# Kernel tuning notes

Measured on AMD Instinct MI355X. Metric: run time of the kernel, lower is better.

## Reference

```python
import jax, jax.numpy as jnp
import numpy as np

HEADS = 4
DIM_HEAD = 32
EPS = 1e-5


def setup_inputs() -> dict:
    key = jax.random.key(0)
    ks = jax.random.split(key, 3)
    b, c, h, w = 32, 128, 128, 128
    hidden = HEADS * DIM_HEAD  # 128
    x = jax.random.normal(ks[0], (b, c, h, w), dtype=jnp.float32)
    Wqkv = jax.random.normal(ks[1], (3 * hidden, c), dtype=jnp.float32) * (1.0 / np.sqrt(c))
    Wout = jax.random.normal(ks[2], (c, hidden), dtype=jnp.float32) * (1.0 / np.sqrt(hidden))
    bout = jnp.zeros((c,), dtype=jnp.float32)
    g = jnp.ones((c,), dtype=jnp.float32)
    return {"x": x, "Wqkv": Wqkv, "Wout": Wout, "bout": bout, "g": g}


def reference(x, Wqkv, Wout, bout, g):
    b, c, h, w = x.shape
    n = h * w
    scale = DIM_HEAD ** -0.5
    # 1x1 conv (no bias) == channel GEMM
    qkv = jnp.einsum('oc,bchw->bohw', Wqkv, x)  # [b, 3*hidden, h, w]
    q, k, v = jnp.split(qkv, 3, axis=1)
    # b (h d) x y -> b h d n
    def to_heads(t):
        return t.reshape(b, HEADS, DIM_HEAD, n)
    q, k, v = to_heads(q), to_heads(k), to_heads(v)
    q = jax.nn.softmax(q, axis=-2) * scale   # softmax over per-head channel dim
    k = jax.nn.softmax(k, axis=-1)           # softmax over token dim
    v = v / n
    ctx = jnp.einsum('bhdn,bhen->bhde', k, v)   # [b, heads, d, e]
    out = jnp.einsum('bhde,bhdn->bhen', ctx, q)  # [b, heads, e, n]
    out = out.reshape(b, HEADS * DIM_HEAD, h, w)
    # output 1x1 conv with bias
    y = jnp.einsum('oc,bchw->bohw', Wout, out) + bout[None, :, None, None]
    # LayerNorm over channel dim (biased variance)
    mean = jnp.mean(y, axis=1, keepdims=True)
    var = jnp.var(y, axis=1, keepdims=True)
    return (y - mean) * jax.lax.rsqrt(var + EPS) * g[None, :, None, None]
```

## Files before the change

kernel.cpp:

```cpp
#include <hip/hip_runtime.h>
#include <math.h>


#define NCHUNK 64

typedef __attribute__((ext_vector_type(8))) short short8;
typedef __attribute__((ext_vector_type(4))) float f32x4;

__device__ __forceinline__ uint bf16r(float f) {
    uint u = __float_as_uint(f);
    return (u + 0x7FFFu + ((u >> 16) & 1u)) >> 16;
}
__device__ __forceinline__ float bf16f(uint h) { return __uint_as_float(h << 16); }
__device__ __forceinline__ uint2 bsplit(float f) {
    uint h = bf16r(f);
    float r = f - bf16f(h);
    return make_uint2(h, bf16r(r));
}
__device__ __forceinline__ uint2 bsplit_t(float f) {
    uint u = __float_as_uint(f);
    uint uh = u & 0xFFFF0000u;
    float r = f - __uint_as_float(uh);
    return make_uint2(uh >> 16, __float_as_uint(r) >> 16);
}
__device__ __forceinline__ uint bpack_t(float f) {
    uint u = __float_as_uint(f);
    uint uh = u & 0xFFFF0000u;
    float r = f - __uint_as_float(uh);
    return (uh >> 16) | (__float_as_uint(r) & 0xFFFF0000u);
}
__device__ __forceinline__ short8 lo8(uint4 a, uint4 b) {
    uint4 r;
    r.x = (a.x & 0xFFFFu) | (a.y << 16);
    r.y = (a.z & 0xFFFFu) | (a.w << 16);
    r.z = (b.x & 0xFFFFu) | (b.y << 16);
    r.w = (b.z & 0xFFFFu) | (b.w << 16);
    return __builtin_bit_cast(short8, r);
}
__device__ __forceinline__ short8 hi8(uint4 a, uint4 b) {
    uint4 r;
    r.x = (a.x >> 16) | (a.y & 0xFFFF0000u);
    r.y = (a.z >> 16) | (a.w & 0xFFFF0000u);
    r.z = (b.x >> 16) | (b.y & 0xFFFF0000u);
    r.w = (b.z >> 16) | (b.w & 0xFFFF0000u);
    return __builtin_bit_cast(short8, r);
}

__global__ __launch_bounds__(256)
void wsplit(const float* __restrict__ W, ushort* __restrict__ Wh,
            ushort* __restrict__ Wl, int n)
{
    const int base = (blockIdx.x * 256 + threadIdx.x) * 4;
    if (base + 3 < n) {
        const float4 f = *(const float4*)(W + base);
        const uint2 a = bsplit(f.x), b2 = bsplit(f.y), c = bsplit(f.z), d = bsplit(f.w);
        ushort4 hh; hh.x = (ushort)a.x; hh.y = (ushort)b2.x; hh.z = (ushort)c.x; hh.w = (ushort)d.x;
        ushort4 ll; ll.x = (ushort)a.y; ll.y = (ushort)b2.y; ll.z = (ushort)c.y; ll.w = (ushort)d.y;
        *(ushort4*)(Wh + base) = hh;
        *(ushort4*)(Wl + base) = ll;
    }
}

#define MFMA(A, B, C) __builtin_amdgcn_mfma_f32_16x16x32_bf16((A), (B), (C), 0, 0, 0)

__global__ __launch_bounds__(512, 1)
void la_k1(const float* __restrict__ x,
           const ushort* __restrict__ Wh, const ushort* __restrict__ Wl,
           float* __restrict__ Spart, float* __restrict__ Zpart)
{
    __shared__ __align__(16) char smb[163840];

    const int tid = threadIdx.x;
    const int b = blockIdx.y, chunk = blockIdx.x;
    const int w = tid >> 6, l = tid & 63;
    const int l15 = l & 15, lg = l >> 4;

    {
#pragma unroll
        for (int it = 0; it < 16; ++it) {
            const int q = tid + 512 * it;
            const int region = q >> 12;
            const int lin = (q & 4095) * 16;
            const int r = lin >> 8;
            const int dst = (region << 16) + (lin ^ ((r & 7) << 4));
            const ushort* src = (region ? Wl : Wh) + 128 * 128 + (lin >> 1);
            *(uint4*)(&smb[dst]) = *(const uint4*)src;
        }
    }

    f32x4 s2[2];
#pragma unroll
    for (int i = 0; i < 2; ++i) s2[i] = (f32x4){0.f, 0.f, 0.f, 0.f};
    float zrow[4];
#pragma unroll
    for (int i = 0; i < 4; ++i) zrow[i] = 0.f;

    const int hh = w >> 1, eh = w & 1;

    for (int t = 0; t < 8; ++t) {
        const int p0 = chunk * 256 + t * 32;
        {
            const float* xb = x + (size_t)b * 128 * 16384 + p0;
            const int cp = tid >> 3, j = tid & 7;
            const int pb = j * 4, c = cp * 2;
            const float4 a = *(const float4*)(xb + (size_t)c * 16384 + pb);
            const float4 bq = *(const float4*)(xb + (size_t)(c + 1) * 16384 + pb);
            const float av[4] = {a.x, a.y, a.z, a.w};
            const float bv[4] = {bq.x, bq.y, bq.z, bq.w};
#pragma unroll
            for (int pp = 0; pp < 4; ++pp) {
                const uint2 s0 = bsplit_t(av[pp]);
                const uint2 s1 = bsplit_t(bv[pp]);
                const int p = pb + pp;
                const int byt = (p * 256 + c * 2) ^ (((p ^ (p >> 3)) & 7) << 4);
                *(uint*)(&smb[131072 + byt])        = s0.x | (s1.x << 16);
                *(uint*)(&smb[131072 + 8192 + byt]) = s0.y | (s1.y << 16);
            }
        }
        __syncthreads();

        f32x4 acc[2][2];
#pragma unroll
        for (int rt = 0; rt < 2; ++rt)
#pragma unroll
            for (int ct = 0; ct < 2; ++ct) acc[rt][ct] = (f32x4){0.f, 0.f, 0.f, 0.f};
#pragma unroll
        for (int ks = 0; ks < 4; ++ks) {
            short8 Bh[2], Bl[2];
#pragma unroll
            for (int ct = 0; ct < 2; ++ct) {
                const int p = ct * 16 + l15;
                const int byt = (p * 256 + (ks * 32 + lg * 8) * 2) ^ (((p ^ (p >> 3)) & 7) << 4);
                Bh[ct] = *(const short8*)(&smb[131072 + byt]);
                Bl[ct] = *(const short8*)(&smb[131072 + 8192 + byt]);
            }
#pragma unroll
            for (int rt = 0; rt < 2; ++rt) {
                const int r = (w + rt * 8) * 16 + l15;
                const int abyt = (r * 256 + (ks * 32 + lg * 8) * 2) ^ ((r & 7) << 4);
                const short8 Ah_ = *(const short8*)(&smb[abyt]);
                const short8 Al_ = *(const short8*)(&smb[65536 + abyt]);
#pragma unroll
                for (int ct = 0; ct < 2; ++ct) {
                    acc[rt][ct] = MFMA(Ah_, Bh[ct], acc[rt][ct]);
                    acc[rt][ct] = MFMA(Ah_, Bl[ct], acc[rt][ct]);
                    acc[rt][ct] = MFMA(Al_, Bh[ct], acc[rt][ct]);
                }
            }
        }
        __syncthreads();

#pragma unroll
        for (int rt = 0; rt < 2; ++rt) {
            const bool isk = (rt == 0);
#pragma unroll
            for (int ct = 0; ct < 2; ++ct) {
                const int p = ct * 16 + l15;
#pragma unroll
                for (int i = 0; i < 4; ++i) {
                    float val = acc[rt][ct][i];
                    if (isk) {
                        val = expf(val);
                        zrow[i] += val;
                    }
                    const int r = w * 16 + lg * 4 + i;
                    const int byt = (r * 128 + p * 4) ^ ((r & 7) << 4);
                    *(uint*)(&smb[131072 + (isk ? 0 : 16384) + byt]) = bpack_t(val);
                }
            }
        }
        __syncthreads();

        {
            short8 A2h[2], A2l[2], B2h, B2l;
#pragma unroll
            for (int rt2 = 0; rt2 < 2; ++rt2) {
                const int r = hh * 32 + rt2 * 16 + l15;
                const int b0 = (r * 128 + lg * 32) ^ ((r & 7) << 4);
                const int b1 = (r * 128 + lg * 32 + 16) ^ ((r & 7) << 4);
                const uint4 q0 = *(const uint4*)(&smb[131072 + b0]);
                const uint4 q1 = *(const uint4*)(&smb[131072 + b1]);
                A2h[rt2] = lo8(q0, q1);
                A2l[rt2] = hi8(q0, q1);
            }
            {
                const int rv = hh * 32 + eh * 16 + l15;
                const int c0 = (rv * 128 + lg * 32) ^ ((rv & 7) << 4);
                const int c1 = (rv * 128 + lg * 32 + 16) ^ ((rv & 7) << 4);
                const uint4 r0 = *(const uint4*)(&smb[131072 + 16384 + c0]);
                const uint4 r1 = *(const uint4*)(&smb[131072 + 16384 + c1]);
                B2h = lo8(r0, r1);
                B2l = hi8(r0, r1);
            }
#pragma unroll
            for (int rt2 = 0; rt2 < 2; ++rt2) {
                s2[rt2] = MFMA(A2h[rt2], B2h, s2[rt2]);
                s2[rt2] = MFMA(A2h[rt2], B2l, s2[rt2]);
                s2[rt2] = MFMA(A2l[rt2], B2h, s2[rt2]);
            }
        }
        __syncthreads();
    }

    const size_t sbase = (((size_t)b * NCHUNK + chunk) * 4 + hh) * 1024;
#pragma unroll
    for (int rt2 = 0; rt2 < 2; ++rt2)
#pragma unroll
        for (int i = 0; i < 4; ++i) {
            const int d = rt2 * 16 + lg * 4 + i;
            const int e = eh * 16 + l15;
            Spart[sbase + d * 32 + e] = s2[rt2][i];
        }

#pragma unroll
    for (int i = 0; i < 4; ++i) {
        float z = zrow[i];
        z += __shfl_xor(z, 1, 64);
        z += __shfl_xor(z, 2, 64);
        z += __shfl_xor(z, 4, 64);
        z += __shfl_xor(z, 8, 64);
        if (l15 == 0)
            Zpart[((size_t)b * NCHUNK + chunk) * 128 + w * 16 + lg * 4 + i] = z;
    }
}

__global__ __launch_bounds__(256, 1)
void la_k1_reduce(const float* __restrict__ Spart, const float* __restrict__ Zpart,
                  float* __restrict__ ctxF)
{
    const int tid = threadIdx.x;
    const int b  = blockIdx.x >> 2;
    const int hh = blockIdx.x & 3;
    const int d  = tid >> 3;
    const int e0 = (tid & 7) << 2;
    float sx = 0.f, sy = 0.f, sz = 0.f, sw = 0.f, z = 0.f;
    for (int ch = 0; ch < NCHUNK; ++ch) {
        const size_t base = (((size_t)b * NCHUNK + ch) * 4 + hh) * 32 + d;
        const float4 v = *(const float4*)(Spart + base * 32 + e0);
        sx += v.x; sy += v.y; sz += v.z; sw += v.w;
        z += Zpart[base];
    }
    const float inv = 1.0f / (z * 16384.0f);
    float4 r; r.x = sx * inv; r.y = sy * inv; r.z = sz * inv; r.w = sw * inv;
    *(float4*)(ctxF + ((((size_t)b * 4 + hh) * 32 + d) << 5) + e0) = r;
}

__global__ __launch_bounds__(256, 1)
void la_mk(const float* __restrict__ Wout, const float* __restrict__ ctxF,
           ushort* __restrict__ Mh, ushort* __restrict__ Ml)
{
    __shared__ float ctxs[4096];
    const int b = blockIdx.x;
    const int tid = threadIdx.x;
#pragma unroll
    for (int i = 0; i < 4; ++i) {
        const int idx = (tid + 256 * i) * 4;
        *(float4*)(ctxs + idx) = *(const float4*)(ctxF + (size_t)b * 4096 + idx);
    }
    __syncthreads();
    const int cp = tid & 127;
    const int dh = tid >> 7;
#pragma unroll
    for (int hq = 0; hq < 2; ++hq) {
        const int h = dh * 2 + hq;
        float wrow[32];
#pragma unroll
        for (int e4 = 0; e4 < 8; ++e4) {
            const float4 wv = *(const float4*)(Wout + cp * 128 + h * 32 + e4 * 4);
            wrow[e4 * 4 + 0] = wv.x; wrow[e4 * 4 + 1] = wv.y;
            wrow[e4 * 4 + 2] = wv.z; wrow[e4 * 4 + 3] = wv.w;
        }
        for (int d = 0; d < 32; ++d) {
            float m = 0.f;
#pragma unroll
            for (int e = 0; e < 32; ++e)
                m += wrow[e] * ctxs[h * 1024 + d * 32 + e];
            const uint2 s = bsplit(m);
            const size_t mo = (size_t)b * 16384 + cp * 128 + h * 32 + d;
            Mh[mo] = (ushort)s.x;
            Ml[mo] = (ushort)s.y;
        }
    }
}

__device__ __forceinline__ int xswz64(int p, int cbyte) {
    return (p * 256 + cbyte) ^ (((p ^ (p >> 3)) & 7) << 4);
}
__device__ __forceinline__ int qswz(int p, int off) {
    return (p * 64 + off) ^ (((p >> 1) & 3) << 4);
}

__global__ __launch_bounds__(256, 4)
void la_k2(const float* __restrict__ x,
           const ushort* __restrict__ Wqh, const ushort* __restrict__ Wql,
           const ushort* __restrict__ Mh, const ushort* __restrict__ Ml,
           const float* __restrict__ bout, const float* __restrict__ g,
           float* __restrict__ outg)
{
    __shared__ __align__(16) char smb[33792];

    const int tid = threadIdx.x;
    const int b = blockIdx.y, chunk = blockIdx.x;
    const int p0 = chunk * 64;
    const int w = tid >> 6, l = tid & 63;
    const int l15 = l & 15, lg = l >> 4;
    const int ch2 = w >> 1;
    const int rp  = w & 1;

    short8 AqH[2][4], AqL[2][4];
#pragma unroll
    for (int t_ = 0; t_ < 2; ++t_)
#pragma unroll
        for (int ks = 0; ks < 4; ++ks) {
            const size_t aoff = (size_t)((2 * w + t_) * 16 + l15) * 128 + ks * 32 + lg * 8;
            AqH[t_][ks] = *(const short8*)(Wqh + aoff);
            AqL[t_][ks] = *(const short8*)(Wql + aoff);
        }

    {
        const float* xb = x + (size_t)b * 128 * 16384 + p0;
        const int j = tid & 15, gq = tid >> 4;
        const int pb = j * 4;
#pragma unroll
        for (int u = 0; u < 2; ++u) {
            const int cb = gq * 4 + u * 64;
            const float4 xv0 = *(const float4*)(xb + (size_t)(cb + 0) * 16384 + pb);
            const float4 xv1 = *(const float4*)(xb + (size_t)(cb + 1) * 16384 + pb);
            const float4 xv2 = *(const float4*)(xb + (size_t)(cb + 2) * 16384 + pb);
            const float4 xv3 = *(const float4*)(xb + (size_t)(cb + 3) * 16384 + pb);
            float rc[4][4];
            rc[0][0] = xv0.x; rc[0][1] = xv0.y; rc[0][2] = xv0.z; rc[0][3] = xv0.w;
            rc[1][0] = xv1.x; rc[1][1] = xv1.y; rc[1][2] = xv1.z; rc[1][3] = xv1.w;
            rc[2][0] = xv2.x; rc[2][1] = xv2.y; rc[2][2] = xv2.z; rc[2][3] = xv2.w;
            rc[3][0] = xv3.x; rc[3][1] = xv3.y; rc[3][2] = xv3.z; rc[3][3] = xv3.w;
#pragma unroll
            for (int pp = 0; pp < 4; ++pp) {
                const uint2 s0 = bsplit_t(rc[0][pp]);
                const uint2 s1 = bsplit_t(rc[1][pp]);
                const uint2 s2u = bsplit_t(rc[2][pp]);
                const uint2 s3 = bsplit_t(rc[3][pp]);
                const int p = pb + pp;
                const int byt = xswz64(p, cb * 2);
                *(uint2*)(&smb[byt])         = make_uint2(s0.x | (s1.x << 16), s2u.x | (s3.x << 16));
                *(uint2*)(&smb[16384 + byt]) = make_uint2(s0.y | (s1.y << 16), s2u.y | (s3.y << 16));
            }
        }
    }
    __syncthreads();

    f32x4 qacc[2][4];
#pragma unroll
    for (int t_ = 0; t_ < 2; ++t_)
#pragma unroll
        for (int ct = 0; ct < 4; ++ct) qacc[t_][ct] = (f32x4){0.f, 0.f, 0.f, 0.f};
#pragma unroll
    for (int ks = 0; ks < 4; ++ks) {
#pragma unroll
        for (int ct = 0; ct < 4; ++ct) {
            const int p = ct * 16 + l15;
            const int byt = xswz64(p, (ks * 32 + lg * 8) * 2);
            const short8 Bh_ = *(const short8*)(&smb[byt]);
            const short8 Bl_ = *(const short8*)(&smb[16384 + byt]);
#pragma unroll
            for (int t_ = 0; t_ < 2; ++t_) {
                qacc[t_][ct] = MFMA(AqH[t_][ks], Bh_, qacc[t_][ct]);
                qacc[t_][ct] = MFMA(AqH[t_][ks], Bl_, qacc[t_][ct]);
                qacc[t_][ct] = MFMA(AqL[t_][ks], Bh_, qacc[t_][ct]);
            }
        }
    }

    float vv[4][2][4];
#pragma unroll
    for (int ct = 0; ct < 4; ++ct) {
        float m = -1e30f;
#pragma unroll
        for (int t_ = 0; t_ < 2; ++t_)
#pragma unroll
            for (int i = 0; i < 4; ++i) {
                vv[ct][t_][i] = qacc[t_][ct][i];
                m = fmaxf(m, vv[ct][t_][i]);
            }
        m = fmaxf(m, __shfl_xor(m, 16, 64));
        m = fmaxf(m, __shfl_xor(m, 32, 64));
        float s = 0.f;
#pragma unroll
        for (int t_ = 0; t_ < 2; ++t_)
#pragma unroll
            for (int i = 0; i < 4; ++i) {
                vv[ct][t_][i] = expf(vv[ct][t_][i] - m);
                s += vv[ct][t_][i];
            }
        s += __shfl_xor(s, 16, 64);
        s += __shfl_xor(s, 32, 64);
        const float inv = 0.17677669529663687f / s;
#pragma unroll
        for (int t_ = 0; t_ < 2; ++t_)
#pragma unroll
            for (int i = 0; i < 4; ++i) vv[ct][t_][i] *= inv;
    }
    __syncthreads();

#pragma unroll
    for (int ct = 0; ct < 4; ++ct) {
        const int p = ct * 16 + l15;
#pragma unroll
        for (int t_ = 0; t_ < 2; ++t_) {
            const uint2 a0 = bsplit_t(vv[ct][t_][0]);
            const uint2 a1 = bsplit_t(vv[ct][t_][1]);
            const uint2 a2 = bsplit_t(vv[ct][t_][2]);
            const uint2 a3 = bsplit_t(vv[ct][t_][3]);
            const int byt = w * 4096 + qswz(p, (t_ * 16 + lg * 4) * 2);
            *(uint2*)(&smb[byt])         = make_uint2(a0.x | (a1.x << 16), a2.x | (a3.x << 16));
            *(uint2*)(&smb[16384 + byt]) = make_uint2(a0.y | (a1.y << 16), a2.y | (a3.y << 16));
        }
    }
    __syncthreads();

    f32x4 yacc[4][2];
#pragma unroll
    for (int jj = 0; jj < 4; ++jj)
#pragma unroll
        for (int ct = 0; ct < 2; ++ct) yacc[jj][ct] = (f32x4){0.f, 0.f, 0.f, 0.f};
#pragma unroll
    for (int ks = 0; ks < 4; ++ks) {
        short8 Bh[2], Bl[2];
#pragma unroll
        for (int ct = 0; ct < 2; ++ct) {
            const int p = ch2 * 32 + ct * 16 + l15;
            const int byt = ks * 4096 + qswz(p, lg * 16);
            Bh[ct] = *(const short8*)(&smb[byt]);
            Bl[ct] = *(const short8*)(&smb[16384 + byt]);
        }
#pragma unroll
        for (int jj = 0; jj < 4; ++jj) {
            const int T = rp + 2 * jj;
            const size_t aoff = (size_t)b * 16384 + (size_t)(T * 16 + l15) * 128 + ks * 32 + lg * 8;
            const short8 Ah_ = *(const short8*)(Mh + aoff);
            const short8 Al_ = *(const short8*)(Ml + aoff);
#pragma unroll
            for (int ct = 0; ct < 2; ++ct) {
                yacc[jj][ct] = MFMA(Ah_, Bh[ct], yacc[jj][ct]);
                yacc[jj][ct] = MFMA(Ah_, Bl[ct], yacc[jj][ct]);
                yacc[jj][ct] = MFMA(Al_, Bh[ct], yacc[jj][ct]);
            }
        }
    }

    float4 bo[4], gv[4];
#pragma unroll
    for (int jj = 0; jj < 4; ++jj) {
        const int rbase = (rp + 2 * jj) * 16 + lg * 4;
        bo[jj] = *(const float4*)(bout + rbase);
        gv[jj] = *(const float4*)(g + rbase);
    }
#pragma unroll
    for (int jj = 0; jj < 4; ++jj)
#pragma unroll
        for (int ct = 0; ct < 2; ++ct) {
            yacc[jj][ct][0] += bo[jj].x;
            yacc[jj][ct][1] += bo[jj].y;
            yacc[jj][ct][2] += bo[jj].z;
            yacc[jj][ct][3] += bo[jj].w;
        }
    float* lnred = (float*)(smb + 32768);
    float sm[2], sq[2];
#pragma unroll
    for (int ct = 0; ct < 2; ++ct) {
        float s = 0.f, q = 0.f;
#pragma unroll
        for (int jj = 0; jj < 4; ++jj)
#pragma unroll
            for (int i = 0; i < 4; ++i) {
                const float yv = yacc[jj][ct][i];
                s += yv; q += yv * yv;
            }
        s += __shfl_xor(s, 16, 64); q += __shfl_xor(q, 16, 64);
        s += __shfl_xor(s, 32, 64); q += __shfl_xor(q, 32, 64);
        sm[ct] = s; sq[ct] = q;
    }
    if (lg == 0) {
#pragma unroll
        for (int ct = 0; ct < 2; ++ct) {
            const int p = ch2 * 32 + ct * 16 + l15;
            lnred[(p * 2 + rp) * 2 + 0] = sm[ct];
            lnred[(p * 2 + rp) * 2 + 1] = sq[ct];
        }
    }
    __syncthreads();
#pragma unroll
    for (int ct = 0; ct < 2; ++ct) {
        const int p = ch2 * 32 + ct * 16 + l15;
        const float st = lnred[(p * 2 + 0) * 2 + 0] + lnred[(p * 2 + 1) * 2 + 0];
        const float qt = lnred[(p * 2 + 0) * 2 + 1] + lnred[(p * 2 + 1) * 2 + 1];
        const float mean = st * (1.0f / 128.0f);
        const float var  = qt * (1.0f / 128.0f) - mean * mean;
        const float rstd = 1.0f / sqrtf(var + 1e-5f);
#pragma unroll
        for (int jj = 0; jj < 4; ++jj) {
            const int rbase = (rp + 2 * jj) * 16 + lg * 4;
            const float gg[4] = {gv[jj].x, gv[jj].y, gv[jj].z, gv[jj].w};
#pragma unroll
            for (int i = 0; i < 4; ++i) {
                const float val = (yacc[jj][ct][i] - mean) * rstd * gg[i];
                outg[((size_t)b * 128 + rbase + i) * 16384 + p0 + p] = val;
            }
        }
    }
}

extern "C" void kernel_launch(void* const* d_in, const int* in_sizes, int n_in,
                              void* d_out, int out_size, void* d_ws, size_t ws_size,
                              hipStream_t stream) {
    const float* x    = (const float*)d_in[0];
    const float* Wqkv = (const float*)d_in[1];
    const float* Wout = (const float*)d_in[2];
    const float* bout = (const float*)d_in[3];
    const float* g    = (const float*)d_in[4];
    float* out = (float*)d_out;

    float* Spart = (float*)d_ws;
    float* Zpart = Spart + (size_t)32 * NCHUNK * 4 * 32 * 32;
    float* ctxF  = Zpart + (size_t)32 * NCHUNK * 4 * 32;
    ushort* Wqh  = (ushort*)(ctxF + (size_t)32 * 4096);
    ushort* Wql  = Wqh + 384 * 128;
    ushort* Mh   = (ushort*)Spart;
    ushort* Ml   = Mh + (size_t)32 * 16384;
    (void)in_sizes; (void)n_in; (void)out_size; (void)ws_size;

    wsplit<<<dim3(48), 256, 0, stream>>>(Wqkv, Wqh, Wql, 384 * 128);
    la_k1<<<dim3(NCHUNK, 32), 512, 0, stream>>>(x, Wqh, Wql, Spart, Zpart);
    la_k1_reduce<<<dim3(128), 256, 0, stream>>>(Spart, Zpart, ctxF);
    la_mk<<<dim3(32), 256, 0, stream>>>(Wout, ctxF, Mh, Ml);
    la_k2<<<dim3(256, 32), 256, 0, stream>>>(x, Wqh, Wql, Mh, Ml, bout, g, out);
}
```

Before: 466.2 us.

## Compute q softmax in first pass and store packed q to workspace

The first pass now also computes the q projection, applies the per-head channel softmax and scale, and writes q as split bf16 pairs to a workspace buffer. A new second-pass kernel reads these precomputed q values instead of re-reading x and recomputing the q projection, then applies the fused M matrix, bias and LayerNorm. The aim is to avoid recomputing the q GEMM in the second pass. The cost is a large extra write and read of q (32*4*16384*32 uints, about 268 MB), plus added register pressure in the first kernel. The new path is used only if the workspace is large enough, otherwise the old path runs.

```diff
diff --git a/kernel.cpp b/kernel.cpp
--- a/kernel.cpp
+++ b/kernel.cpp
@@ -66,7 +66,8 @@
 __global__ __launch_bounds__(512, 1)
 void la_k1(const float* __restrict__ x,
            const ushort* __restrict__ Wh, const ushort* __restrict__ Wl,
-           float* __restrict__ Spart, float* __restrict__ Zpart)
+           float* __restrict__ Spart, float* __restrict__ Zpart,
+           uint* __restrict__ qsG)
 {
     __shared__ __align__(16) char smb[163840];
 
@@ -74,6 +75,8 @@
     const int b = blockIdx.y, chunk = blockIdx.x;
     const int w = tid >> 6, l = tid & 63;
     const int l15 = l & 15, lg = l >> 4;
+    const bool doq = (qsG != nullptr);
+    const int hq = w >> 1, qct = w & 1;
 
     {
 #pragma unroll
@@ -86,6 +89,17 @@
             const ushort* src = (region ? Wl : Wh) + 128 * 128 + (lin >> 1);
             *(uint4*)(&smb[dst]) = *(const uint4*)src;
         }
+    }
+    short8 AqH[2][4], AqL[2][4];
+    if (doq) {
+#pragma unroll
+        for (int t_ = 0; t_ < 2; ++t_)
+#pragma unroll
+            for (int ks = 0; ks < 4; ++ks) {
+                const size_t aoff = (size_t)((2 * hq + t_) * 16 + l15) * 128 + ks * 32 + lg * 8;
+                AqH[t_][ks] = *(const short8*)(Wh + aoff);
+                AqL[t_][ks] = *(const short8*)(Wl + aoff);
+            }
     }
 
     f32x4 s2[2];
@@ -124,6 +138,9 @@
         for (int rt = 0; rt < 2; ++rt)
 #pragma unroll
             for (int ct = 0; ct < 2; ++ct) acc[rt][ct] = (f32x4){0.f, 0.f, 0.f, 0.f};
+        f32x4 qacc[2];
+        qacc[0] = (f32x4){0.f, 0.f, 0.f, 0.f};
+        qacc[1] = (f32x4){0.f, 0.f, 0.f, 0.f};
 #pragma unroll
         for (int ks = 0; ks < 4; ++ks) {
             short8 Bh[2], Bl[2];
@@ -145,6 +162,14 @@
                     acc[rt][ct] = MFMA(Ah_, Bh[ct], acc[rt][ct]);
                     acc[rt][ct] = MFMA(Ah_, Bl[ct], acc[rt][ct]);
                     acc[rt][ct] = MFMA(Al_, Bh[ct], acc[rt][ct]);
+                }
+            }
+            if (doq) {
+#pragma unroll
+                for (int t_ = 0; t_ < 2; ++t_) {
+                    qacc[t_] = MFMA(AqH[t_][ks], Bh[qct], qacc[t_]);
+                    qacc[t_] = MFMA(AqH[t_][ks], Bl[qct], qacc[t_]);
+                    qacc[t_] = MFMA(AqL[t_][ks], Bh[qct], qacc[t_]);
                 }
             }
         }
@@ -197,6 +222,42 @@
                 s2[rt2] = MFMA(A2h[rt2], B2h, s2[rt2]);
                 s2[rt2] = MFMA(A2h[rt2], B2l, s2[rt2]);
                 s2[rt2] = MFMA(A2l[rt2], B2h, s2[rt2]);
+            }
+        }
+
+        if (doq) {
+            float vv[2][4];
+            float m = -1e30f;
+#pragma unroll
+            for (int t_ = 0; t_ < 2; ++t_)
+#pragma unroll
+                for (int i = 0; i < 4; ++i) {
+                    vv[t_][i] = qacc[t_][i];
+                    m = fmaxf(m, vv[t_][i]);
+                }
+            m = fmaxf(m, __shfl_xor(m, 16, 64));
+            m = fmaxf(m, __shfl_xor(m, 32, 64));
+            float s = 0.f;
+#pragma unroll
+            for (int t_ = 0; t_ < 2; ++t_)
+#pragma unroll
+                for (int i = 0; i < 4; ++i) {
+                    vv[t_][i] = expf(vv[t_][i] - m);
+                    s += vv[t_][i];
+                }
+            s += __shfl_xor(s, 16, 64);
+            s += __shfl_xor(s, 32, 64);
+            const float inv = 0.17677669529663687f / s;
+            const int pg = p0 + qct * 16 + l15;
+            uint* qp = qsG + ((size_t)(b * 4 + hq) * 16384 + pg) * 32;
+#pragma unroll
+            for (int t_ = 0; t_ < 2; ++t_) {
+                uint4 pk;
+                pk.x = bpack_t(vv[t_][0] * inv);
+                pk.y = bpack_t(vv[t_][1] * inv);
+                pk.z = bpack_t(vv[t_][2] * inv);
+                pk.w = bpack_t(vv[t_][3] * inv);
+                *(uint4*)(qp + t_ * 16 + lg * 4) = pk;
             }
         }
         __syncthreads();
@@ -283,6 +344,78 @@
     }
 }
 
+__global__ __launch_bounds__(256, 4)
+void la_k2f(const uint* __restrict__ qsG,
+            const ushort* __restrict__ Mh, const ushort* __restrict__ Ml,
+            const float* __restrict__ bout, const float* __restrict__ g,
+            float* __restrict__ outg)
+{
+    const int tid = threadIdx.x;
+    const int b = blockIdx.y, chunk = blockIdx.x;
+    const int w = tid >> 6, l = tid & 63;
+    const int l15 = l & 15, lg = l >> 4;
+    const int p = chunk * 64 + w * 16 + l15;
+
+    short8 Bh[4], Bl[4];
+#pragma unroll
+    for (int h = 0; h < 4; ++h) {
+        const uint* qp = qsG + ((size_t)(b * 4 + h) * 16384 + p) * 32 + lg * 8;
+        const uint4 r0 = *(const uint4*)qp;
+        const uint4 r1 = *(const uint4*)(qp + 4);
+        Bh[h] = lo8(r0, r1);
+        Bl[h] = hi8(r0, r1);
+    }
+
+    f32x4 yacc[8];
+#pragma unroll
+    for (int T = 0; T < 8; ++T) yacc[T] = (f32x4){0.f, 0.f, 0.f, 0.f};
+#pragma unroll
+    for (int ks = 0; ks < 4; ++ks) {
+#pragma unroll
+        for (int T = 0; T < 8; ++T) {
+            const size_t aoff = (size_t)b * 16384 + (size_t)(T * 16 + l15) * 128 + ks * 32 + lg * 8;
+            const short8 Ah_ = *(const short8*)(Mh + aoff);
+            const short8 Al_ = *(const short8*)(Ml + aoff);
+            yacc[T] = MFMA(Ah_, Bh[ks], yacc[T]);
+            yacc[T] = MFMA(Ah_, Bl[ks], yacc[T]);
+            yacc[T] = MFMA(Al_, Bh[ks], yacc[T]);
+        }
+    }
+
+    float4 bo[8], gv[8];
+#pragma unroll
+    for (int T = 0; T < 8; ++T) {
+        bo[T] = *(const float4*)(bout + T * 16 + lg * 4);
+        gv[T] = *(const float4*)(g + T * 16 + lg * 4);
+    }
+    float s = 0.f, q = 0.f;
+#pragma unroll
+    for (int T = 0; T < 8; ++T) {
+        yacc[T][0] += bo[T].x; yacc[T][1] += bo[T].y;
+        yacc[T][2] += bo[T].z; yacc[T][3] += bo[T].w;
+#pragma unroll
+        for (int i = 0; i < 4; ++i) {
+            const float yv = yacc[T][i];
+            s += yv; q += yv * yv;
+        }
+    }
+    s += __shfl_xor(s, 16, 64); q += __shfl_xor(q, 16, 64);
+    s += __shfl_xor(s, 32, 64); q += __shfl_xor(q, 32, 64);
+    const float mean = s * (1.0f / 128.0f);
+    const float var  = q * (1.0f / 128.0f) - mean * mean;
+    const float rstd = 1.0f / sqrtf(var + 1e-5f);
+
+#pragma unroll
+    for (int T = 0; T < 8; ++T) {
+        const float gg[4] = {gv[T].x, gv[T].y, gv[T].z, gv[T].w};
+#pragma unroll
+        for (int i = 0; i < 4; ++i) {
+            const int o = T * 16 + lg * 4 + i;
+            outg[((size_t)b * 128 + o) * 16384 + p] = (yacc[T][i] - mean) * rstd * gg[i];
+        }
+    }
+}
+
 __device__ __forceinline__ int xswz64(int p, int cbyte) {
     return (p * 256 + cbyte) ^ (((p ^ (p >> 3)) & 7) << 4);
 }
@@ -524,13 +657,21 @@
     float* ctxF  = Zpart + (size_t)32 * NCHUNK * 4 * 32;
     ushort* Wqh  = (ushort*)(ctxF + (size_t)32 * 4096);
     ushort* Wql  = Wqh + 384 * 128;
+    uint*  qsG   = (uint*)(Wql + 384 * 128);
     ushort* Mh   = (ushort*)Spart;
     ushort* Ml   = Mh + (size_t)32 * 16384;
-    (void)in_sizes; (void)n_in; (void)out_size; (void)ws_size;
+    (void)in_sizes; (void)n_in; (void)out_size;
+
+    const size_t need = (size_t)((char*)(qsG + (size_t)32 * 4 * 16384 * 32) - (char*)d_ws);
+    const bool fused = ws_size >= need;
 
     wsplit<<<dim3(48), 256, 0, stream>>>(Wqkv, Wqh, Wql, 384 * 128);
-    la_k1<<<dim3(NCHUNK, 32), 512, 0, stream>>>(x, Wqh, Wql, Spart, Zpart);
+    la_k1<<<dim3(NCHUNK, 32), 512, 0, stream>>>(x, Wqh, Wql, Spart, Zpart,
+                                                fused ? qsG : (uint*)nullptr);
     la_k1_reduce<<<dim3(128), 256, 0, stream>>>(Spart, Zpart, ctxF);
     la_mk<<<dim3(32), 256, 0, stream>>>(Wout, ctxF, Mh, Ml);
-    la_k2<<<dim3(256, 32), 256, 0, stream>>>(x, Wqh, Wql, Mh, Ml, bout, g, out);
-}
+    if (fused)
+        la_k2f<<<dim3(256, 32), 256, 0, stream>>>(qsG, Mh, Ml, bout, g, out);
+    else
+        la_k2<<<dim3(256, 32), 256, 0, stream>>>(x, Wqh, Wql, Mh, Ml, bout, g, out);
+}
```

Result: slower. 1.080 ms (+131.7%).
